# Kernel tuning notes

Hardware: AMD Instinct MI355X
Metric: run time of the kernel (lower is better)

Reference implementation:

```python
import jax, jax.numpy as jnp
import numpy as np

N_NODES = 100000
N_EDGES = 1250000
N_GRAPHS = 256
IN_DIM, HID, OUT = 7, 64, 2


def setup_inputs() -> dict:
    key = jax.random.key(0)
    ks = jax.random.split(key, 10)
    x = jax.random.normal(ks[0], (N_NODES, IN_DIM), dtype=jnp.float32)
    edge_index = jax.random.randint(ks[1], (2, N_EDGES), 0, N_NODES, dtype=jnp.int64)
    batch = jnp.sort(jax.random.randint(ks[2], (N_NODES,), 0, N_GRAPHS, dtype=jnp.int64))
    def glorot(k, shape):
        lim = float(np.sqrt(6.0 / (shape[0] + shape[1])))
        return jax.random.uniform(k, shape, jnp.float32, -lim, lim)
    return {
        "x": x, "edge_index": edge_index, "batch": batch,
        "W1": glorot(ks[3], (IN_DIM, HID)), "b1": jnp.zeros((HID,), jnp.float32),
        "W2": glorot(ks[4], (HID, HID)),   "b2": jnp.zeros((HID,), jnp.float32),
        "W3": glorot(ks[5], (HID, HID)),   "b3": jnp.zeros((HID,), jnp.float32),
        "Wl": glorot(ks[6], (HID, OUT)),   "bl": jnp.zeros((OUT,), jnp.float32),
    }


def _gcn_conv(x, src, dst, W, b, n_nodes):
    # PyG GCNConv: add self-loops, symmetric deg^{-1/2} normalization,
    # linear transform, scatter-add aggregation at target nodes, + bias.
    deg = jax.ops.segment_sum(jnp.ones_like(dst, dtype=x.dtype), dst, num_segments=n_nodes)
    dinv = jnp.where(deg > 0, jax.lax.rsqrt(deg), 0.0)
    norm = dinv[src] * dinv[dst]                      # [E+N]
    h = x @ W                                         # [N, out]
    msg = h[src] * norm[:, None]                      # gather + scale
    out = jax.ops.segment_sum(msg, dst, num_segments=n_nodes)
    return out + b


def reference(x, edge_index, batch, W1, b1, W2, b2, W3, b3, Wl, bl):
    n = x.shape[0]
    loop = jnp.arange(n, dtype=edge_index.dtype)
    src = jnp.concatenate([edge_index[0], loop])      # self-loops appended once
    dst = jnp.concatenate([edge_index[1], loop])

    h = jax.nn.relu(_gcn_conv(x, src, dst, W1, b1, n))
    h = jax.nn.relu(_gcn_conv(h, src, dst, W2, b2, n))
    h = _gcn_conv(h, src, dst, W3, b3, n)

    # global_mean_pool over graphs
    sums = jax.ops.segment_sum(h, batch, num_segments=N_GRAPHS)
    cnt = jax.ops.segment_sum(jnp.ones((n,), h.dtype), batch, num_segments=N_GRAPHS)
    pooled = sums / jnp.maximum(cnt, 1.0)[:, None]    # [G, HID]

    # dropout is identity in eval mode
    return pooled @ Wl + bl                           # [G, 2]
```

## Files before the change

kernel.cpp:

```cpp
#include <hip/hip_runtime.h>
#include <hip/hip_fp16.h>

#define HID 64
#define NGRAPHS 256
#define CHUNK 4096
#define BKTSZ 512
#define BKTSH 9
#define PSH 17
#define PMASK 0x1FFFF

typedef _Float16 half8 __attribute__((ext_vector_type(8)));
typedef float f32x4 __attribute__((ext_vector_type(4)));



__global__ __launch_bounds__(256) void k_hist(
        const int* __restrict__ dst, const float* __restrict__ W2,
        const float* __restrict__ W3, __half* __restrict__ Wf2,
        __half* __restrict__ Wf3, int* __restrict__ H,
        float* __restrict__ gsum, int e, int nbkt, int nchunk) {
    __shared__ int cnt4[4][256];
    const int t = threadIdx.x, b = blockIdx.x;
    const int gtid = b * 256 + t;
    if (gtid < 512) {
        int p = gtid;
        int kt = p >> 8, c = (p >> 6) & 3, lane = p & 63;
        int quad = lane >> 4, m = lane & 15;
#pragma unroll
        for (int j = 0; j < 8; ++j) {
            int k = kt * 32 + quad * 8 + j;
            int ch = c * 16 + m;
            Wf2[(size_t)p * 8 + j] = __float2half(W2[k * HID + ch]);
            Wf3[(size_t)p * 8 + j] = __float2half(W3[k * HID + ch]);
        }
    }
    if (b == 0) {
        for (int i = t; i < NGRAPHS * HID; i += 256) gsum[i] = 0.0f;
    }
    for (int i = t; i < 1024; i += 256) ((int*)cnt4)[i] = 0;
    __syncthreads();
    const int w = t >> 6;
#pragma unroll
    for (int it = 0; it < CHUNK / 1024; ++it) {
        int idx = b * CHUNK + it * 1024 + t * 4;
        if (idx + 3 < e) {
            int4 d = *(const int4*)(dst + idx);
            atomicAdd(&cnt4[w][d.x >> BKTSH], 1);
            atomicAdd(&cnt4[w][d.y >> BKTSH], 1);
            atomicAdd(&cnt4[w][d.z >> BKTSH], 1);
            atomicAdd(&cnt4[w][d.w >> BKTSH], 1);
        } else {
            for (int i = idx; i < e && i < idx + 4; ++i)
                atomicAdd(&cnt4[w][dst[i] >> BKTSH], 1);
        }
    }
    __syncthreads();
    for (int i = t; i < nbkt; i += 256)
        H[i * nchunk + b] = cnt4[0][i] + cnt4[1][i] + cnt4[2][i] + cnt4[3][i];
}


__global__ __launch_bounds__(256) void k_scan(const int* __restrict__ in,
                                              int* __restrict__ outp,
                                              int* __restrict__ bsum, int n) {
    __shared__ int sh[256];
    const int t = threadIdx.x;
    const int base = blockIdx.x * 1024 + t * 4;
    int v[4];
    int s = 0;
#pragma unroll
    for (int k = 0; k < 4; k++) {
        int i = base + k;
        v[k] = (i < n) ? in[i] : 0;
        s += v[k];
    }
    sh[t] = s;
    __syncthreads();
#pragma unroll
    for (int off = 1; off < 256; off <<= 1) {
        int add = (t >= off) ? sh[t - off] : 0;
        __syncthreads();
        sh[t] += add;
        __syncthreads();
    }
    int run = sh[t] - s;
#pragma unroll
    for (int k = 0; k < 4; k++) {
        int i = base + k;
        if (i < n) outp[i] = run;
        run += v[k];
    }
    if (t == 255) bsum[blockIdx.x] = sh[255];
}


__global__ __launch_bounds__(256) void k_scatter(
        const int* __restrict__ src, const int* __restrict__ dst,
        const int* __restrict__ Hs, const int* __restrict__ bsum,
        int* __restrict__ packed, int e, int nbkt, int nchunk, int nscan) {
    __shared__ int off[256];
    __shared__ int lc[256];
    __shared__ int bscan[64];
    const int t = threadIdx.x, b = blockIdx.x;
    if (t < 64) bscan[t] = (t < nscan) ? bsum[t] : 0;
    __syncthreads();
#pragma unroll
    for (int o = 1; o < 64; o <<= 1) {
        int add = (t < 64 && t >= o) ? bscan[t - o] : 0;
        __syncthreads();
        if (t < 64) bscan[t] += add;
        __syncthreads();
    }
    for (int i = t; i < nbkt; i += 256) {
        int idx = i * nchunk + b;
        int q = idx >> 10;
        off[i] = Hs[idx] + (q ? bscan[q - 1] : 0);
        lc[i] = 0;
    }
    __syncthreads();
#pragma unroll
    for (int it = 0; it < CHUNK / 1024; ++it) {
        int idx = b * CHUNK + it * 1024 + t * 4;
        if (idx + 3 < e) {
            int4 d = *(const int4*)(dst + idx);
            int4 s = *(const int4*)(src + idx);
            int b0 = d.x >> BKTSH, b1 = d.y >> BKTSH;
            int b2 = d.z >> BKTSH, b3 = d.w >> BKTSH;
            int r0 = atomicAdd(&lc[b0], 1);
            int r1 = atomicAdd(&lc[b1], 1);
            int r2 = atomicAdd(&lc[b2], 1);
            int r3 = atomicAdd(&lc[b3], 1);
            packed[off[b0] + r0] = s.x | ((d.x & (BKTSZ - 1)) << PSH);
            packed[off[b1] + r1] = s.y | ((d.y & (BKTSZ - 1)) << PSH);
            packed[off[b2] + r2] = s.z | ((d.z & (BKTSZ - 1)) << PSH);
            packed[off[b3] + r3] = s.w | ((d.w & (BKTSZ - 1)) << PSH);
        } else {
            for (int i = idx; i < e && i < idx + 4; ++i) {
                int dd = dst[i];
                int bk = dd >> BKTSH;
                int r = atomicAdd(&lc[bk], 1);
                packed[off[bk] + r] = src[i] | ((dd & (BKTSZ - 1)) << PSH);
            }
        }
    }
}


__global__ __launch_bounds__(256) void k_csr_build(
        const int* __restrict__ packed, const int* __restrict__ Hs,
        const int* __restrict__ bsum, int* __restrict__ rowptr,
        float* __restrict__ dinv, int* __restrict__ csr,
        const float* __restrict__ x, float* __restrict__ xt,
        int e, int n, int nbkt, int nchunk, int nscan) {
    __shared__ int cnt[BKTSZ];
    __shared__ int pref[BKTSZ];
    __shared__ int ssum[256];
    __shared__ int cnt2[BKTSZ];
    __shared__ int bscan[64];
    const int t = threadIdx.x, bkt = blockIdx.x;
    if (t < 64) bscan[t] = (t < nscan) ? bsum[t] : 0;
    if (bkt == 0 && t == 0) rowptr[n] = e;
    cnt[t] = 0; cnt[t + 256] = 0;
    cnt2[t] = 0; cnt2[t + 256] = 0;
    __syncthreads();
#pragma unroll
    for (int o = 1; o < 64; o <<= 1) {
        int add = (t < 64 && t >= o) ? bscan[t - o] : 0;
        __syncthreads();
        if (t < 64) bscan[t] += add;
        __syncthreads();
    }
    int i0 = bkt * nchunk;
    int q0 = i0 >> 10;
    int segStart = Hs[i0] + (q0 ? bscan[q0 - 1] : 0);
    int segEnd = e;
    if (bkt + 1 < nbkt) {
        int i1 = (bkt + 1) * nchunk;
        int q1 = i1 >> 10;
        segEnd = Hs[i1] + (q1 ? bscan[q1 - 1] : 0);
    }
    for (int j = segStart + t; j < segEnd; j += 256)
        atomicAdd(&cnt[(packed[j] >> PSH) & (BKTSZ - 1)], 1);
    __syncthreads();
    int a0 = cnt[2 * t], a1 = cnt[2 * t + 1];
    int s = a0 + a1;
    ssum[t] = s;
    __syncthreads();
#pragma unroll
    for (int off = 1; off < 256; off <<= 1) {
        int add = (t >= off) ? ssum[t - off] : 0;
        __syncthreads();
        ssum[t] += add;
        __syncthreads();
    }
    int p = ssum[t] - s;
    pref[2 * t] = p;
    pref[2 * t + 1] = p + a0;
    __syncthreads();
    for (int i = t; i < BKTSZ; i += 256) {
        int node = bkt * BKTSZ + i;
        if (node < n) {
            rowptr[node] = segStart + pref[i];
            dinv[node] = rsqrtf((float)(cnt[i] + 1));
        }
    }
    for (int j = segStart + t; j < segEnd; j += 256) {
        int pk = packed[j];
        int ld = (pk >> PSH) & (BKTSZ - 1);
        int r = atomicAdd(&cnt2[ld], 1);
        csr[segStart + pref[ld] + r] = pk & PMASK;
    }
    for (int i = t; i < BKTSZ * 8; i += 256) {
        int nl = i >> 3, k = i & 7;
        int node = bkt * BKTSZ + nl;
        if (node < n)
            xt[(size_t)node * 8 + k] =
                (k < 7) ? x[(size_t)node * 7 + k] * rsqrtf((float)(cnt[nl] + 1))
                        : 0.0f;
    }
}

__device__ __forceinline__ float4 h4_to_f4(int2 raw) {
    __half2 p0 = *(__half2*)&raw.x;
    __half2 p1 = *(__half2*)&raw.y;
    float2 f0 = __half22float2(p0);
    float2 f1 = __half22float2(p1);
    return make_float4(f0.x, f0.y, f1.x, f1.y);
}


__global__ __launch_bounds__(256) void k_aggx_gemm(
        const int* __restrict__ rowptr, const int* __restrict__ csr,
        const float* __restrict__ xt, const float* __restrict__ b,
        const float* __restrict__ dinv, const float* __restrict__ W1,
        const __half* __restrict__ Wf, __half* __restrict__ hout,
        int n_nodes) {
    __shared__ __half act[16 * 72];
    __shared__ float W1s[7 * HID];
    const int t = threadIdx.x;
    const int n0 = blockIdx.x * 16;
    const int nl = t >> 4;
    const int node = n0 + nl;
    const int l16 = t & 15;
    const int c8 = l16 & 7;
    const float4* b4 = (const float4*)b;

    for (int i = t; i < 7 * HID; i += 256) W1s[i] = W1[i];

    float4 av = make_float4(0.0f, 0.0f, 0.0f, 0.0f);
    if (node < n_nodes) {
        int beg = rowptr[node], end = rowptr[node + 1];
        float dv = dinv[node];
        float inner = (l16 < 8) ? xt[(size_t)node * 8 + c8] : 0.0f;
        int j = beg;
        for (; j + 7 < end; j += 8) {
            int e8 = csr[j + c8];
            int sid[4];
#pragma unroll
            for (int q = 0; q < 4; ++q)
                sid[q] = __shfl(e8, 2 * q + (l16 >> 3), 8);
            float r[4];
#pragma unroll
            for (int q = 0; q < 4; ++q)
                r[q] = xt[(size_t)sid[q] * 8 + c8];
#pragma unroll
            for (int q = 0; q < 4; ++q) inner += r[q];
        }
        if (j + 3 < end) {
            int e4 = csr[j + (l16 & 3)];
            int sid[2];
#pragma unroll
            for (int q = 0; q < 2; ++q)
                sid[q] = __shfl(e4, 2 * q + (l16 >> 3), 4);
            float r[2];
#pragma unroll
            for (int q = 0; q < 2; ++q)
                r[q] = xt[(size_t)sid[q] * 8 + c8];
            inner += r[0] + r[1];
            j += 4;
        }
        for (; j < end; ++j)
            if (l16 < 8) inner += xt[(size_t)csr[j] * 8 + c8];

        inner += __shfl_xor(inner, 8, 16);
        float agg[7];
#pragma unroll
        for (int k = 0; k < 7; ++k) agg[k] = __shfl(inner, k, 16);

        float4 bb = b4[l16];
#pragma unroll
        for (int i = 0; i < 4; ++i) {
            int c = l16 * 4 + i;
            float dot = 0.0f;
#pragma unroll
            for (int k = 0; k < 7; ++k) dot += agg[k] * W1s[k * HID + c];
            float v = ((const float*)&bb)[i] + dv * dot;
            ((float*)&av)[i] = fmaxf(v, 0.0f);
        }
    }
    {
        __half2 p0 = __floats2half2_rn(av.x, av.y);
        __half2 p1 = __floats2half2_rn(av.z, av.w);
        int2 pk;
        pk.x = *(int*)&p0;
        pk.y = *(int*)&p1;
        *(int2*)&act[nl * 72 + l16 * 4] = pk;
    }
    __syncthreads();

    const int wave = t >> 6, lane = t & 63;
    const int quad = lane >> 4, m = lane & 15;
    const half8* Wf8 = (const half8*)Wf;
    f32x4 acc = {0.0f, 0.0f, 0.0f, 0.0f};
#pragma unroll
    for (int kt = 0; kt < 2; ++kt) {
        half8 a = *(const half8*)&act[m * 72 + kt * 32 + quad * 8];
        half8 bv = Wf8[(kt * 4 + wave) * 64 + lane];
        acc = __builtin_amdgcn_mfma_f32_16x16x32_f16(a, bv, acc, 0, 0, 0);
    }
#pragma unroll
    for (int r = 0; r < 4; ++r) {
        int nd = n0 + quad * 4 + r;
        if (nd < n_nodes)
            hout[(size_t)nd * HID + wave * 16 + m] =
                __float2half(acc[r] * dinv[nd]);
    }
}


__global__ __launch_bounds__(256) void k_agg_gemm(
        const int* __restrict__ rowptr, const int* __restrict__ csr,
        const __half* __restrict__ h, const float* __restrict__ b,
        const float* __restrict__ dinv, const __half* __restrict__ Wf,
        __half* __restrict__ hout, int n_nodes) {
    __shared__ __half act[16 * 72];
    const int t = threadIdx.x;
    const int n0 = blockIdx.x * 16;
    const int nl = t >> 4;
    const int node = n0 + nl;
    const int l16 = t & 15;
    const int2* h8 = (const int2*)h;
    const float4* b4 = (const float4*)b;

    float4 av = make_float4(0.0f, 0.0f, 0.0f, 0.0f);
    if (node < n_nodes) {
        int beg = rowptr[node], end = rowptr[node + 1];
        float dv = dinv[node];
        float4 inner = h4_to_f4(h8[(size_t)node * 16 + l16]);
        int j = beg;
        for (; j + 7 < end; j += 8) {
            int e8 = csr[j + (l16 & 7)];
            int2 r[8];
#pragma unroll
            for (int q = 0; q < 8; ++q)
                r[q] = h8[(size_t)__shfl(e8, q, 8) * 16 + l16];
#pragma unroll
            for (int q = 0; q < 8; ++q) {
                float4 v = h4_to_f4(r[q]);
                inner.x += v.x; inner.y += v.y; inner.z += v.z; inner.w += v.w;
            }
        }
        if (j + 3 < end) {
            int e4 = csr[j + (l16 & 3)];
            int2 r[4];
#pragma unroll
            for (int q = 0; q < 4; ++q)
                r[q] = h8[(size_t)__shfl(e4, q, 4) * 16 + l16];
#pragma unroll
            for (int q = 0; q < 4; ++q) {
                float4 v = h4_to_f4(r[q]);
                inner.x += v.x; inner.y += v.y; inner.z += v.z; inner.w += v.w;
            }
            j += 4;
        }
        for (; j < end; j++) {
            float4 v = h4_to_f4(h8[(size_t)csr[j] * 16 + l16]);
            inner.x += v.x; inner.y += v.y; inner.z += v.z; inner.w += v.w;
        }
        float4 bb = b4[l16];
        av.x = fmaxf(bb.x + dv * inner.x, 0.0f);
        av.y = fmaxf(bb.y + dv * inner.y, 0.0f);
        av.z = fmaxf(bb.z + dv * inner.z, 0.0f);
        av.w = fmaxf(bb.w + dv * inner.w, 0.0f);
    }
    {
        __half2 p0 = __floats2half2_rn(av.x, av.y);
        __half2 p1 = __floats2half2_rn(av.z, av.w);
        int2 pk;
        pk.x = *(int*)&p0;
        pk.y = *(int*)&p1;
        *(int2*)&act[nl * 72 + l16 * 4] = pk;
    }
    __syncthreads();

    const int wave = t >> 6, lane = t & 63;
    const int quad = lane >> 4, m = lane & 15;
    const half8* Wf8 = (const half8*)Wf;
    f32x4 acc = {0.0f, 0.0f, 0.0f, 0.0f};
#pragma unroll
    for (int kt = 0; kt < 2; ++kt) {
        half8 a = *(const half8*)&act[m * 72 + kt * 32 + quad * 8];
        half8 bv = Wf8[(kt * 4 + wave) * 64 + lane];
        acc = __builtin_amdgcn_mfma_f32_16x16x32_f16(a, bv, acc, 0, 0, 0);
    }
#pragma unroll
    for (int r = 0; r < 4; ++r) {
        int nd = n0 + quad * 4 + r;
        if (nd < n_nodes)
            hout[(size_t)nd * HID + wave * 16 + m] =
                __float2half(acc[r] * dinv[nd]);
    }
}


__global__ __launch_bounds__(256) void k_agg_part(
        const int* __restrict__ rowptr, const int* __restrict__ csr,
        const __half* __restrict__ h, const float* __restrict__ b,
        const float* __restrict__ dinv, const int* __restrict__ batch,
        float* __restrict__ partv, int* __restrict__ partg,
        float* __restrict__ gsum, int n_nodes) {
    __shared__ float redbuf[16][64];
    __shared__ int bg[16];
    const int t = threadIdx.x;
    const int n0 = blockIdx.x * 16;
    const int nl = t >> 4;
    const int node = n0 + nl;
    const int l16 = t & 15;
    const int2* h8 = (const int2*)h;
    const float4* b4 = (const float4*)b;

    if (t < 16) {
        int nd = n0 + t;
        bg[t] = (nd < n_nodes) ? batch[nd] : -1;
    }

    float4 res = make_float4(0.0f, 0.0f, 0.0f, 0.0f);
    if (node < n_nodes) {
        int beg = rowptr[node], end = rowptr[node + 1];
        float dv = dinv[node];
        float4 inner = h4_to_f4(h8[(size_t)node * 16 + l16]);
        int j = beg;
        for (; j + 7 < end; j += 8) {
            int e8 = csr[j + (l16 & 7)];
            int2 r[8];
#pragma unroll
            for (int q = 0; q < 8; ++q)
                r[q] = h8[(size_t)__shfl(e8, q, 8) * 16 + l16];
#pragma unroll
            for (int q = 0; q < 8; ++q) {
                float4 v = h4_to_f4(r[q]);
                inner.x += v.x; inner.y += v.y; inner.z += v.z; inner.w += v.w;
            }
        }
        if (j + 3 < end) {
            int e4 = csr[j + (l16 & 3)];
            int2 r[4];
#pragma unroll
            for (int q = 0; q < 4; ++q)
                r[q] = h8[(size_t)__shfl(e4, q, 4) * 16 + l16];
#pragma unroll
            for (int q = 0; q < 4; ++q) {
                float4 v = h4_to_f4(r[q]);
                inner.x += v.x; inner.y += v.y; inner.z += v.z; inner.w += v.w;
            }
            j += 4;
        }
        for (; j < end; j++) {
            float4 v = h4_to_f4(h8[(size_t)csr[j] * 16 + l16]);
            inner.x += v.x; inner.y += v.y; inner.z += v.z; inner.w += v.w;
        }
        float4 bb = b4[l16];
        res.x = bb.x + dv * inner.x;
        res.y = bb.y + dv * inner.y;
        res.z = bb.z + dv * inner.z;
        res.w = bb.w + dv * inner.w;
    }
    *(float4*)&redbuf[nl][l16 * 4] = res;
    __syncthreads();

    if (t < 64) {
        const int c = t;
        const int g0 = bg[0];
        const int g15 = bg[15];
        float s0 = 0.0f, s1 = 0.0f;
        for (int i = 0; i < 16; ++i) {
            int g = bg[i];
            float v = redbuf[i][c];
            if (g == g0) s0 += v;
            else if (g == g15) s1 += v;
            else if (g >= 0) atomicAdd(&gsum[g * HID + c], v);
        }
        partv[(size_t)blockIdx.x * 128 + c] = s0;
        partv[(size_t)blockIdx.x * 128 + 64 + c] = s1;
        if (c == 0) {
            partg[blockIdx.x * 2 + 0] = g0;
            partg[blockIdx.x * 2 + 1] = (g15 != g0) ? g15 : -1;
        }
    }
}


__global__ __launch_bounds__(256) void k_pool_head(
        const float* __restrict__ partv, const int* __restrict__ partg,
        const float* __restrict__ gsum, const int* __restrict__ batch,
        const float* __restrict__ Wl, const float* __restrict__ bl,
        float* __restrict__ out, int n_nodes) {
    int g = blockIdx.x;
    int lo = 0, hi = n_nodes;
    while (lo < hi) { int m = (lo + hi) >> 1; if (batch[m] < g) lo = m + 1; else hi = m; }
    int nstart = lo;
    hi = n_nodes;
    while (lo < hi) { int m = (lo + hi) >> 1; if (batch[m] < g + 1) lo = m + 1; else hi = m; }
    int nend = lo;

    int c = threadIdx.x & 63, part = threadIdx.x >> 6;
    float acc = 0.0f;
    if (nend > nstart) {
        int b0 = nstart >> 4, b1 = (nend - 1) >> 4;
        for (int b = b0 + part; b <= b1; b += 4) {
            if (partg[b * 2 + 0] == g) acc += partv[(size_t)b * 128 + c];
            if (partg[b * 2 + 1] == g) acc += partv[(size_t)b * 128 + 64 + c];
        }
    }

    __shared__ float red[4][64];
    __shared__ float hd[128];
    red[part][c] = acc;
    __syncthreads();
    if (threadIdx.x < 64) {
        float cntf = (float)(nend - nstart);
        float pooled = (red[0][c] + red[1][c] + red[2][c] + red[3][c]
                        + gsum[g * HID + c]) / fmaxf(cntf, 1.0f);
        hd[c] = pooled * Wl[c * 2 + 0];
        hd[64 + c] = pooled * Wl[c * 2 + 1];
    }
    __syncthreads();
    if (threadIdx.x < 2) {
        float s = 0.0f;
        for (int k = 0; k < 64; k++) s += hd[threadIdx.x * 64 + k];
        out[g * 2 + threadIdx.x] = s + bl[threadIdx.x];
    }
}


extern "C" void kernel_launch(void* const* d_in, const int* in_sizes, int n_in,
                              void* d_out, int out_size, void* d_ws, size_t ws_size,
                              hipStream_t stream) {
    const float* x     = (const float*)d_in[0];
    const int*   ei    = (const int*)d_in[1];
    const int*   batch = (const int*)d_in[2];
    const float* W1    = (const float*)d_in[3];
    const float* b1    = (const float*)d_in[4];
    const float* W2    = (const float*)d_in[5];
    const float* b2    = (const float*)d_in[6];
    const float* W3    = (const float*)d_in[7];
    const float* b3    = (const float*)d_in[8];
    const float* Wl    = (const float*)d_in[9];
    const float* bl    = (const float*)d_in[10];
    float* out = (float*)d_out;

    const int N = in_sizes[0] / 7;
    const int E = in_sizes[1] / 2;
    const int* src = ei;
    const int* dst = ei + E;

    const int nbkt   = (N + BKTSZ - 1) >> BKTSH;
    const int nchunk = (E + CHUNK - 1) / CHUNK;
    const int lenH   = nbkt * nchunk;
    const int nscan  = (lenH + 1023) / 1024;

    char* ws = (char*)d_ws;
    size_t off = 0;
    auto carve = [&](size_t bytes) {
        void* p = ws + off;
        off = (off + bytes + 255) & ~(size_t)255;
        return p;
    };
    int*    H      = (int*)carve((size_t)lenH * 4);
    int*    Hs     = (int*)carve((size_t)lenH * 4);
    int*    bsum   = (int*)carve(512 * 4);
    int*    packed = (int*)carve((size_t)E * 4);
    int*    csr    = (int*)carve((size_t)E * 4);
    int*    rowptr = (int*)carve((size_t)(N + 1) * 4);
    float*  dinv   = (float*)carve((size_t)N * 4);
    __half* Wf2    = (__half*)carve(4096 * 2);
    __half* Wf3    = (__half*)carve(4096 * 2);
    float*  gsum   = (float*)carve((size_t)NGRAPHS * HID * 4);
    float*  xt     = (float*)carve((size_t)(N + 64) * 8 * 4);
    __half* bufH   = (__half*)carve((size_t)(N + 64) * HID * 2);
    __half* bufB   = (__half*)carve((size_t)(N + 64) * HID * 2);

    const int nb_agg = (N + 15) / 16;
    float* partv = (float*)carve((size_t)nb_agg * 128 * 4);
    int*   partg = (int*)carve((size_t)nb_agg * 2 * 4);

    k_hist<<<nchunk, 256, 0, stream>>>(dst, W2, W3, Wf2, Wf3, H, gsum,
                                       E, nbkt, nchunk);
    k_scan<<<nscan, 256, 0, stream>>>(H, Hs, bsum, lenH);
    k_scatter<<<nchunk, 256, 0, stream>>>(src, dst, Hs, bsum, packed,
                                          E, nbkt, nchunk, nscan);
    k_csr_build<<<nbkt, 256, 0, stream>>>(packed, Hs, bsum, rowptr, dinv, csr,
                                          x, xt, E, N, nbkt, nchunk, nscan);

    k_aggx_gemm<<<nb_agg, 256, 0, stream>>>(rowptr, csr, xt, b1, dinv, W1,
                                            Wf2, bufB, N);
    k_agg_gemm<<<nb_agg, 256, 0, stream>>>(rowptr, csr, bufB, b2, dinv, Wf3, bufH, N);
    k_agg_part<<<nb_agg, 256, 0, stream>>>(rowptr, csr, bufH, b3, dinv, batch,
                                           partv, partg, gsum, N);

    k_pool_head<<<NGRAPHS, 256, 0, stream>>>(partv, partg, gsum, batch,
                                             Wl, bl, out, N);
}
```

Measured before the change: 222.8 us.

## Fold final linear head into layer-3 weights to aggregate 2-dim features

Since the third GCN layer, mean pooling and the final linear head are all linear, W3·Wl is precomputed into a 64x2 matrix. The layer-2 aggregation kernel then projects each node straight to 2 values instead of running a 64-wide MFMA GEMM. The third aggregation gathers 8-byte float2 per edge instead of 128-byte fp16 rows, and the b3 contribution is added analytically in the head. This removes most of the gather traffic of the last layer, but changes the floating-point summation order.

Measured after the change: 196.8 us. 1.13x faster.

```diff
diff --git a/kernel.cpp b/kernel.cpp
--- a/kernel.cpp
+++ b/kernel.cpp
@@ -16,9 +16,10 @@
 
 __global__ __launch_bounds__(256) void k_hist(
         const int* __restrict__ dst, const float* __restrict__ W2,
-        const float* __restrict__ W3, __half* __restrict__ Wf2,
-        __half* __restrict__ Wf3, int* __restrict__ H,
-        float* __restrict__ gsum, int e, int nbkt, int nchunk) {
+        const float* __restrict__ W3, const float* __restrict__ Wl,
+        __half* __restrict__ Wf2, float* __restrict__ W3l,
+        int* __restrict__ H, float* __restrict__ gsum,
+        int e, int nbkt, int nchunk) {
     __shared__ int cnt4[4][256];
     const int t = threadIdx.x, b = blockIdx.x;
     const int gtid = b * 256 + t;
@@ -31,11 +32,17 @@
             int k = kt * 32 + quad * 8 + j;
             int ch = c * 16 + m;
             Wf2[(size_t)p * 8 + j] = __float2half(W2[k * HID + ch]);
-            Wf3[(size_t)p * 8 + j] = __float2half(W3[k * HID + ch]);
         }
     }
     if (b == 0) {
-        for (int i = t; i < NGRAPHS * HID; i += 256) gsum[i] = 0.0f;
+        for (int i = t; i < NGRAPHS * 2; i += 256) gsum[i] = 0.0f;
+        if (t < 128) {
+            int j = t >> 1, o = t & 1;
+            float s = 0.0f;
+#pragma unroll
+            for (int k = 0; k < HID; ++k) s += W3[j * HID + k] * Wl[k * 2 + o];
+            W3l[j * 2 + o] = s;
+        }
     }
     for (int i = t; i < 1024; i += 256) ((int*)cnt4)[i] = 0;
     __syncthreads();
@@ -328,12 +335,11 @@
 }
 
 
-__global__ __launch_bounds__(256) void k_agg_gemm(
+__global__ __launch_bounds__(256) void k_agg_z(
         const int* __restrict__ rowptr, const int* __restrict__ csr,
         const __half* __restrict__ h, const float* __restrict__ b,
-        const float* __restrict__ dinv, const __half* __restrict__ Wf,
-        __half* __restrict__ hout, int n_nodes) {
-    __shared__ __half act[16 * 72];
+        const float* __restrict__ dinv, const float* __restrict__ W3l,
+        float2* __restrict__ zbuf, int n_nodes) {
     const int t = threadIdx.x;
     const int n0 = blockIdx.x * 16;
     const int nl = t >> 4;
@@ -342,10 +348,18 @@
     const int2* h8 = (const int2*)h;
     const float4* b4 = (const float4*)b;
 
+    float w3l0[4], w3l1[4];
+#pragma unroll
+    for (int i = 0; i < 4; ++i) {
+        w3l0[i] = W3l[(l16 * 4 + i) * 2 + 0];
+        w3l1[i] = W3l[(l16 * 4 + i) * 2 + 1];
+    }
+
     float4 av = make_float4(0.0f, 0.0f, 0.0f, 0.0f);
+    float dv = 0.0f;
     if (node < n_nodes) {
         int beg = rowptr[node], end = rowptr[node + 1];
-        float dv = dinv[node];
+        dv = dinv[node];
         float4 inner = h4_to_f4(h8[(size_t)node * 16 + l16]);
         int j = beg;
         for (; j + 7 < end; j += 8) {
@@ -383,119 +397,84 @@
         av.z = fmaxf(bb.z + dv * inner.z, 0.0f);
         av.w = fmaxf(bb.w + dv * inner.w, 0.0f);
     }
-    {
-        __half2 p0 = __floats2half2_rn(av.x, av.y);
-        __half2 p1 = __floats2half2_rn(av.z, av.w);
-        int2 pk;
-        pk.x = *(int*)&p0;
-        pk.y = *(int*)&p1;
-        *(int2*)&act[nl * 72 + l16 * 4] = pk;
-    }
-    __syncthreads();
-
-    const int wave = t >> 6, lane = t & 63;
-    const int quad = lane >> 4, m = lane & 15;
-    const half8* Wf8 = (const half8*)Wf;
-    f32x4 acc = {0.0f, 0.0f, 0.0f, 0.0f};
-#pragma unroll
-    for (int kt = 0; kt < 2; ++kt) {
-        half8 a = *(const half8*)&act[m * 72 + kt * 32 + quad * 8];
-        half8 bv = Wf8[(kt * 4 + wave) * 64 + lane];
-        acc = __builtin_amdgcn_mfma_f32_16x16x32_f16(a, bv, acc, 0, 0, 0);
-    }
-#pragma unroll
-    for (int r = 0; r < 4; ++r) {
-        int nd = n0 + quad * 4 + r;
-        if (nd < n_nodes)
-            hout[(size_t)nd * HID + wave * 16 + m] =
-                __float2half(acc[r] * dinv[nd]);
-    }
-}
-
-
-__global__ __launch_bounds__(256) void k_agg_part(
+    float p0 = av.x * w3l0[0] + av.y * w3l0[1] + av.z * w3l0[2] + av.w * w3l0[3];
+    float p1 = av.x * w3l1[0] + av.y * w3l1[1] + av.z * w3l1[2] + av.w * w3l1[3];
+#pragma unroll
+    for (int o = 8; o; o >>= 1) {
+        p0 += __shfl_xor(p0, o, 16);
+        p1 += __shfl_xor(p1, o, 16);
+    }
+    if (node < n_nodes && l16 == 0)
+        zbuf[node] = make_float2(p0 * dv, p1 * dv);
+}
+
+
+__global__ __launch_bounds__(256) void k_zagg_part(
         const int* __restrict__ rowptr, const int* __restrict__ csr,
-        const __half* __restrict__ h, const float* __restrict__ b,
-        const float* __restrict__ dinv, const int* __restrict__ batch,
-        float* __restrict__ partv, int* __restrict__ partg,
-        float* __restrict__ gsum, int n_nodes) {
-    __shared__ float redbuf[16][64];
+        const float2* __restrict__ zbuf, const float* __restrict__ dinv,
+        const int* __restrict__ batch, float* __restrict__ partv,
+        int* __restrict__ partg, float* __restrict__ gsum, int n_nodes) {
+    __shared__ float2 ys[16];
     __shared__ int bg[16];
     const int t = threadIdx.x;
     const int n0 = blockIdx.x * 16;
     const int nl = t >> 4;
     const int node = n0 + nl;
-    const int l16 = t & 15;
-    const int2* h8 = (const int2*)h;
-    const float4* b4 = (const float4*)b;
+    const int q = t & 15;
 
     if (t < 16) {
         int nd = n0 + t;
         bg[t] = (nd < n_nodes) ? batch[nd] : -1;
     }
 
-    float4 res = make_float4(0.0f, 0.0f, 0.0f, 0.0f);
+    float2 yv = make_float2(0.0f, 0.0f);
     if (node < n_nodes) {
         int beg = rowptr[node], end = rowptr[node + 1];
+        float2 acc = make_float2(0.0f, 0.0f);
+        if (q == 0) acc = zbuf[node];
+        int j = beg;
+        for (; j + 15 < end; j += 16) {
+            int e = csr[j + q];
+            float2 v = zbuf[e];
+            acc.x += v.x; acc.y += v.y;
+        }
+        int rem = end - j;
+        if (q < rem) {
+            int e = csr[j + q];
+            float2 v = zbuf[e];
+            acc.x += v.x; acc.y += v.y;
+        }
+#pragma unroll
+        for (int o = 8; o; o >>= 1) {
+            acc.x += __shfl_xor(acc.x, o, 16);
+            acc.y += __shfl_xor(acc.y, o, 16);
+        }
         float dv = dinv[node];
-        float4 inner = h4_to_f4(h8[(size_t)node * 16 + l16]);
-        int j = beg;
-        for (; j + 7 < end; j += 8) {
-            int e8 = csr[j + (l16 & 7)];
-            int2 r[8];
-#pragma unroll
-            for (int q = 0; q < 8; ++q)
-                r[q] = h8[(size_t)__shfl(e8, q, 8) * 16 + l16];
-#pragma unroll
-            for (int q = 0; q < 8; ++q) {
-                float4 v = h4_to_f4(r[q]);
-                inner.x += v.x; inner.y += v.y; inner.z += v.z; inner.w += v.w;
-            }
-        }
-        if (j + 3 < end) {
-            int e4 = csr[j + (l16 & 3)];
-            int2 r[4];
-#pragma unroll
-            for (int q = 0; q < 4; ++q)
-                r[q] = h8[(size_t)__shfl(e4, q, 4) * 16 + l16];
-#pragma unroll
-            for (int q = 0; q < 4; ++q) {
-                float4 v = h4_to_f4(r[q]);
-                inner.x += v.x; inner.y += v.y; inner.z += v.z; inner.w += v.w;
-            }
-            j += 4;
-        }
-        for (; j < end; j++) {
-            float4 v = h4_to_f4(h8[(size_t)csr[j] * 16 + l16]);
-            inner.x += v.x; inner.y += v.y; inner.z += v.z; inner.w += v.w;
-        }
-        float4 bb = b4[l16];
-        res.x = bb.x + dv * inner.x;
-        res.y = bb.y + dv * inner.y;
-        res.z = bb.z + dv * inner.z;
-        res.w = bb.w + dv * inner.w;
-    }
-    *(float4*)&redbuf[nl][l16 * 4] = res;
-    __syncthreads();
-
-    if (t < 64) {
-        const int c = t;
+        yv = make_float2(acc.x * dv, acc.y * dv);
+    }
+    if (q == 0) ys[nl] = yv;
+    __syncthreads();
+
+    if (t == 0) {
         const int g0 = bg[0];
         const int g15 = bg[15];
-        float s0 = 0.0f, s1 = 0.0f;
+        float2 s0 = make_float2(0.0f, 0.0f), s1 = make_float2(0.0f, 0.0f);
         for (int i = 0; i < 16; ++i) {
             int g = bg[i];
-            float v = redbuf[i][c];
-            if (g == g0) s0 += v;
-            else if (g == g15) s1 += v;
-            else if (g >= 0) atomicAdd(&gsum[g * HID + c], v);
-        }
-        partv[(size_t)blockIdx.x * 128 + c] = s0;
-        partv[(size_t)blockIdx.x * 128 + 64 + c] = s1;
-        if (c == 0) {
-            partg[blockIdx.x * 2 + 0] = g0;
-            partg[blockIdx.x * 2 + 1] = (g15 != g0) ? g15 : -1;
-        }
+            float2 v = ys[i];
+            if (g == g0) { s0.x += v.x; s0.y += v.y; }
+            else if (g == g15) { s1.x += v.x; s1.y += v.y; }
+            else if (g >= 0) {
+                atomicAdd(&gsum[g * 2 + 0], v.x);
+                atomicAdd(&gsum[g * 2 + 1], v.y);
+            }
+        }
+        partv[(size_t)blockIdx.x * 4 + 0] = s0.x;
+        partv[(size_t)blockIdx.x * 4 + 1] = s0.y;
+        partv[(size_t)blockIdx.x * 4 + 2] = s1.x;
+        partv[(size_t)blockIdx.x * 4 + 3] = s1.y;
+        partg[blockIdx.x * 2 + 0] = g0;
+        partg[blockIdx.x * 2 + 1] = (g15 != g0) ? g15 : -1;
     }
 }
 
@@ -503,8 +482,8 @@
 __global__ __launch_bounds__(256) void k_pool_head(
         const float* __restrict__ partv, const int* __restrict__ partg,
         const float* __restrict__ gsum, const int* __restrict__ batch,
-        const float* __restrict__ Wl, const float* __restrict__ bl,
-        float* __restrict__ out, int n_nodes) {
+        const float* __restrict__ b3, const float* __restrict__ Wl,
+        const float* __restrict__ bl, float* __restrict__ out, int n_nodes) {
     int g = blockIdx.x;
     int lo = 0, hi = n_nodes;
     while (lo < hi) { int m = (lo + hi) >> 1; if (batch[m] < g) lo = m + 1; else hi = m; }
@@ -513,32 +492,28 @@
     while (lo < hi) { int m = (lo + hi) >> 1; if (batch[m] < g + 1) lo = m + 1; else hi = m; }
     int nend = lo;
 
-    int c = threadIdx.x & 63, part = threadIdx.x >> 6;
-    float acc = 0.0f;
+    const int t = threadIdx.x;
+    float ax = 0.0f, ay = 0.0f;
     if (nend > nstart) {
         int b0 = nstart >> 4, b1 = (nend - 1) >> 4;
-        for (int b = b0 + part; b <= b1; b += 4) {
-            if (partg[b * 2 + 0] == g) acc += partv[(size_t)b * 128 + c];
-            if (partg[b * 2 + 1] == g) acc += partv[(size_t)b * 128 + 64 + c];
-        }
-    }
-
-    __shared__ float red[4][64];
-    __shared__ float hd[128];
-    red[part][c] = acc;
-    __syncthreads();
-    if (threadIdx.x < 64) {
-        float cntf = (float)(nend - nstart);
-        float pooled = (red[0][c] + red[1][c] + red[2][c] + red[3][c]
-                        + gsum[g * HID + c]) / fmaxf(cntf, 1.0f);
-        hd[c] = pooled * Wl[c * 2 + 0];
-        hd[64 + c] = pooled * Wl[c * 2 + 1];
-    }
-    __syncthreads();
-    if (threadIdx.x < 2) {
-        float s = 0.0f;
-        for (int k = 0; k < 64; k++) s += hd[threadIdx.x * 64 + k];
-        out[g * 2 + threadIdx.x] = s + bl[threadIdx.x];
+        for (int b = b0 + t; b <= b1; b += 256) {
+            if (partg[b * 2 + 0] == g) { ax += partv[(size_t)b * 4 + 0]; ay += partv[(size_t)b * 4 + 1]; }
+            if (partg[b * 2 + 1] == g) { ax += partv[(size_t)b * 4 + 2]; ay += partv[(size_t)b * 4 + 3]; }
+        }
+    }
+    __shared__ float rx[256], ry[256];
+    rx[t] = ax; ry[t] = ay;
+    __syncthreads();
+    for (int s2 = 128; s2; s2 >>= 1) {
+        if (t < s2) { rx[t] += rx[t + s2]; ry[t] += ry[t + s2]; }
+        __syncthreads();
+    }
+    if (t < 2) {
+        float cntf = fmaxf((float)(nend - nstart), 1.0f);
+        float s = ((t == 0) ? rx[0] : ry[0]) + gsum[g * 2 + t];
+        float hb = 0.0f;
+        for (int c = 0; c < HID; ++c) hb += b3[c] * Wl[c * 2 + t];
+        out[g * 2 + t] = s / cntf + hb + bl[t];
     }
 }
 
@@ -584,17 +559,17 @@
     int*    rowptr = (int*)carve((size_t)(N + 1) * 4);
     float*  dinv   = (float*)carve((size_t)N * 4);
     __half* Wf2    = (__half*)carve(4096 * 2);
-    __half* Wf3    = (__half*)carve(4096 * 2);
-    float*  gsum   = (float*)carve((size_t)NGRAPHS * HID * 4);
+    float*  W3l    = (float*)carve(128 * 4);
+    float*  gsum   = (float*)carve((size_t)NGRAPHS * 2 * 4);
     float*  xt     = (float*)carve((size_t)(N + 64) * 8 * 4);
-    __half* bufH   = (__half*)carve((size_t)(N + 64) * HID * 2);
     __half* bufB   = (__half*)carve((size_t)(N + 64) * HID * 2);
+    float2* zbuf   = (float2*)carve((size_t)(N + 64) * 8);
 
     const int nb_agg = (N + 15) / 16;
-    float* partv = (float*)carve((size_t)nb_agg * 128 * 4);
+    float* partv = (float*)carve((size_t)nb_agg * 4 * 4);
     int*   partg = (int*)carve((size_t)nb_agg * 2 * 4);
 
-    k_hist<<<nchunk, 256, 0, stream>>>(dst, W2, W3, Wf2, Wf3, H, gsum,
+    k_hist<<<nchunk, 256, 0, stream>>>(dst, W2, W3, Wl, Wf2, W3l, H, gsum,
                                        E, nbkt, nchunk);
     k_scan<<<nscan, 256, 0, stream>>>(H, Hs, bsum, lenH);
     k_scatter<<<nchunk, 256, 0, stream>>>(src, dst, Hs, bsum, packed,
@@ -604,10 +579,11 @@
 
     k_aggx_gemm<<<nb_agg, 256, 0, stream>>>(rowptr, csr, xt, b1, dinv, W1,
                                             Wf2, bufB, N);
-    k_agg_gemm<<<nb_agg, 256, 0, stream>>>(rowptr, csr, bufB, b2, dinv, Wf3, bufH, N);
-    k_agg_part<<<nb_agg, 256, 0, stream>>>(rowptr, csr, bufH, b3, dinv, batch,
-                                           partv, partg, gsum, N);
+    k_agg_z<<<nb_agg, 256, 0, stream>>>(rowptr, csr, bufB, b2, dinv, W3l,
+                                        zbuf, N);
+    k_zagg_part<<<nb_agg, 256, 0, stream>>>(rowptr, csr, zbuf, dinv, batch,
+                                            partv, partg, gsum, N);
 
     k_pool_head<<<NGRAPHS, 256, 0, stream>>>(partv, partg, gsum, batch,
-                                             Wl, bl, out, N);
-}
+                                             b3, Wl, bl, out, N);
+}
```
